# Optimization experiments

Hardware: AMD Instinct MI355X
Metric: run time of the kernel (lower is better)

## Reference

```python
import jax, jax.numpy as jnp
import numpy as np

B, S, D = 2, 2048, 1024
H, HD = 16, 64          # num_heads, head_dim
K = 32                  # JL n_components


def setup_inputs() -> dict:
    key = jax.random.key(0)
    k1, k2, k3, k4 = jax.random.split(key, 4)
    return {
        "hidden_states": jax.random.normal(k1, (B, S, D), dtype=jnp.float32),
        "W_attn": jax.random.normal(k2, (D, 3 * D), dtype=jnp.float32) * 0.02,
        "b_attn": jnp.zeros((3 * D,), dtype=jnp.float32),
        "S_proj": jax.random.normal(k3, (K, HD), dtype=jnp.float32) / np.sqrt(K),
        "W_proj": jax.random.normal(k4, (D, D), dtype=jnp.float32) * 0.02,
        "b_proj": jnp.zeros((D,), dtype=jnp.float32),
    }


def reference(hidden_states, W_attn, b_attn, S_proj, W_proj, b_proj):
    b, s, d = hidden_states.shape
    # GPT2 Conv1D: x @ W + b, then split into q,k,v
    qkv = hidden_states @ W_attn + b_attn            # [B,S,3D]
    q, k, v = jnp.split(qkv, 3, axis=-1)
    # split heads -> [B,H,S,HD]
    def split_heads(x):
        return x.reshape(b, s, H, HD).transpose(0, 2, 1, 3)
    q = split_heads(q) @ S_proj.T                    # [B,H,S,K] JL-reduced
    k = split_heads(k) @ S_proj.T                    # [B,H,S,K]
    v = split_heads(v)                               # [B,H,S,HD]
    # naive attention: scale by sqrt(value head_dim) per GPT2 _attn
    scores = jnp.einsum("bhqk,bhsk->bhqs", q, k) / jnp.sqrt(
        jnp.asarray(HD, dtype=v.dtype))              # [B,H,S,S]
    causal = jnp.tril(jnp.ones((s, s), dtype=bool))
    mask_value = jnp.finfo(scores.dtype).min
    scores = jnp.where(causal, scores, mask_value)
    attn = jax.nn.softmax(scores, axis=-1)
    out = jnp.einsum("bhqs,bhsd->bhqd", attn, v)     # [B,H,S,HD]
    out = out.transpose(0, 2, 1, 3).reshape(b, s, d)  # merge heads
    return out @ W_proj + b_proj
```

## Files before the change

### kernel.cpp

```cpp
#include <hip/hip_runtime.h>
#include <hip/hip_bf16.h>
#include <stdint.h>

#define B_ 2
#define S_ 2048
#define D_ 1024
#define H_ 16
#define HD_ 64
#define KJL 32
#define N3 3072
#define N2 2048

typedef __attribute__((ext_vector_type(8))) __bf16 bf16x8;
typedef __attribute__((ext_vector_type(4))) float floatx4;
typedef __attribute__((ext_vector_type(4))) short short4v;
typedef __attribute__((ext_vector_type(2))) unsigned int uint2v;

__device__ __forceinline__ unsigned short f2b(float x) {
  union { float f; unsigned u; } v; v.f = x;
  unsigned r = v.u + 0x7fffu + ((v.u >> 16) & 1u);
  return (unsigned short)(r >> 16);
}

__device__ __forceinline__ unsigned int pkbf(float lo, float hi) {
  union { float f; unsigned u; } a, b;
  a.f = lo; b.f = hi;
  return __builtin_amdgcn_perm(b.u + 0x8000u, a.u + 0x8000u, 0x07060302u);
}

__device__ __forceinline__ void async16(const void* g, void* l) {
  __builtin_amdgcn_global_load_lds((__attribute__((address_space(1))) void*)(g),
                                   (__attribute__((address_space(3))) void*)(l),
                                   16, 0, 0);
}

__global__ __launch_bounds__(256)
void prep_kernel(const float* __restrict__ hidden, unsigned short* __restrict__ hB,
                 const float* __restrict__ W_attn, const float* __restrict__ b_attn,
                 const float* __restrict__ Sp, const float* __restrict__ W_proj,
                 unsigned short* __restrict__ Bt2, unsigned short* __restrict__ WpT,
                 float* __restrict__ bias2) {
  __shared__ float shmem[2048];
  const int bid = blockIdx.x;
  const int tid = threadIdx.x;

  if (bid < 512) {
    const int n4 = (B_ * S_ * D_) / 4;
    int i = bid * 256 + tid;
    for (; i < n4; i += 512 * 256) {
      float4 v = *(const float4*)(hidden + 4 * (size_t)i);
      short4v o = {(short)f2b(v.x), (short)f2b(v.y), (short)f2b(v.z), (short)f2b(v.w)};
      *(short4v*)(hB + 4 * (size_t)i) = o;
    }
  } else if (bid < 2560) {
    const float* in;
    unsigned short* out;
    int Cs, local;
    if (bid < 1536) { local = bid - 512;  in = W_attn + 2048; out = Bt2 + 1024 * 1024; Cs = N3; }
    else            { local = bid - 1536; in = W_proj;        out = WpT;               Cs = D_; }
    float (*t)[33] = (float(*)[33])shmem;
    int c0 = (local & 31) * 32, r0 = (local >> 5) * 32;
    int tx = tid & 31, ty = tid >> 5;
    for (int j = 0; j < 32; j += 8)
      t[ty + j][tx] = in[(size_t)(r0 + ty + j) * Cs + c0 + tx];
    __syncthreads();
    for (int j = 0; j < 32; j += 8)
      out[(size_t)(c0 + ty + j) * D_ + r0 + tx] = f2b(t[tx][ty + j]);
  } else {
    const int lb = bid - 2560;
    const int part = lb >> 6;
    const int h = (lb >> 2) & 15;
    const int dc = lb & 3;
    for (int i = tid; i < 32 * 64; i += 256) shmem[i] = Sp[i];
    __syncthreads();
    const float scale = part ? 1.0f : 0.125f * 1.44269504f;
    const int d = dc * 256 + tid;
    float w[64];
    const float* src = W_attn + (size_t)d * N3 + part * D_ + h * 64;
    for (int j = 0; j < 16; ++j) {
      float4 v = *(const float4*)&src[j * 4];
      w[j * 4 + 0] = v.x; w[j * 4 + 1] = v.y; w[j * 4 + 2] = v.z; w[j * 4 + 3] = v.w;
    }
    const int nbase = part * 512 + h * 32;
    for (int kjl = 0; kjl < 32; ++kjl) {
      float acc = 0.f;
      for (int hd = 0; hd < 64; ++hd) acc += w[hd] * shmem[kjl * 64 + hd];
      Bt2[(size_t)(nbase + kjl) * D_ + d] = f2b(acc * scale);
    }
    if (dc == 0 && tid < 32) {
      float acc = 0.f;
      for (int hd = 0; hd < 64; ++hd) acc += b_attn[part * D_ + h * 64 + hd] * shmem[tid * 64 + hd];
      bias2[nbase + tid] = acc * scale;
    }
  }
}

__global__ __launch_bounds__(256, 2)
void qkv2_gemm_kernel(const unsigned short* __restrict__ A,
                      const unsigned short* __restrict__ Bt,
                      const float* __restrict__ b_attn,
                      const float* __restrict__ bias2,
                      unsigned short* __restrict__ Qjl,
                      unsigned short* __restrict__ Kjl,
                      unsigned short* __restrict__ Vc) {
  __shared__ __align__(16) unsigned short As[2][128 * 32];
  __shared__ __align__(16) unsigned short Bs[2][128 * 32];
  const int tid = threadIdx.x;
  const int lane = tid & 63, wv = tid >> 6;
  const int quad = lane >> 4, col = lane & 15;
  const int wm = wv >> 1, wn = wv & 1;
  const int m0 = blockIdx.y * 128, n0 = blockIdx.x * 128;

  floatx4 acc[4][4] = {};

  for (int kk = 0; kk < D_; kk += 64) {
    for (int it = 0; it < 4; ++it) {
      int c = it * 256 + tid;
      int ks = c >> 9, row = (c >> 2) & 127, kc = c & 3;
      async16(A + (size_t)(m0 + row) * D_ + kk + ks * 32 + kc * 8,
              (unsigned short*)As + c * 8);
    }
    for (int it = 0; it < 4; ++it) {
      int c = it * 256 + tid;
      int ks = c >> 9, row = (c >> 2) & 127, kc = c & 3;
      async16(Bt + (size_t)(n0 + row) * D_ + kk + ks * 32 + kc * 8,
              (unsigned short*)Bs + c * 8);
    }
    asm volatile("s_waitcnt vmcnt(0)" ::: "memory");
    __syncthreads();
    for (int ks = 0; ks < 2; ++ks) {
      bf16x8 af[4], bfr[4];
      for (int mt = 0; mt < 4; ++mt)
        af[mt] = *(const bf16x8*)&As[ks][(wm * 64 + mt * 16 + col) * 32 + quad * 8];
      for (int nt = 0; nt < 4; ++nt)
        bfr[nt] = *(const bf16x8*)&Bs[ks][(wn * 64 + nt * 16 + col) * 32 + quad * 8];
      for (int mt = 0; mt < 4; ++mt)
        for (int nt = 0; nt < 4; ++nt)
          acc[mt][nt] = __builtin_amdgcn_mfma_f32_16x16x32_bf16(
              af[mt], bfr[nt], acc[mt][nt], 0, 0, 0);
    }
    __syncthreads();
  }

  const int pq = n0 >> 9;
  for (int mt = 0; mt < 4; ++mt) {
    int gm0 = m0 + wm * 64 + mt * 16 + quad * 4;
    int b = gm0 >> 11, s = gm0 & (S_ - 1);
    for (int nt = 0; nt < 4; ++nt) {
      int gn = n0 + wn * 64 + nt * 16 + col;
      if (pq >= 2) {
        int vcol = gn - 1024;
        float bs = b_attn[2048 + vcol];
        int h = vcol >> 6, hd = vcol & 63;
        short4v vv;
        for (int i = 0; i < 4; ++i)
          vv[i] = (short)f2b(acc[mt][nt][i] + bs);
        size_t idx = ((((size_t)(b * H_ + h) * 64 + (s >> 5)) * 64 + hd) * 32 + (s & 31));
        *(short4v*)&Vc[idx] = vv;
      } else {
        float bs = bias2[gn];
        int gl = gn & 511;
        int h = gl >> 5, kjl = gl & 31;
        unsigned short* dst = pq ? Kjl : Qjl;
        size_t base = ((size_t)(b * H_ + h) * S_ + s) * KJL + kjl;
        for (int i = 0; i < 4; ++i)
          dst[base + (size_t)i * KJL] = f2b(acc[mt][nt][i] + bs);
      }
    }
  }
}

__global__ __launch_bounds__(256, 1)
void attn_kernel(const unsigned short* __restrict__ Qjl,
                 const unsigned short* __restrict__ Kjl,
                 const unsigned short* __restrict__ Vc,
                 unsigned short* __restrict__ AO) {
  __shared__ __align__(16) unsigned short Kb[3][4096];
  __shared__ __align__(16) unsigned short Vb[3][8192];
  __shared__ __align__(16) unsigned short Ps[4][4096];
  const int tid = threadIdx.x;
  const int lane = tid & 63, wv = tid >> 6;
  const int quad = lane >> 4, l15 = lane & 15;

  const int blk = blockIdx.x;
  const int bh = blk & 31;
  const int u = blk >> 5;
  const int b = bh >> 4, h = bh & 15;

  const unsigned short* Kg = Kjl + (size_t)bh * S_ * KJL;
  const unsigned short* Vg = Vc + (size_t)bh * (64 * 64 * 32);

  char* Pw = (char*)&Ps[wv][0];
  const int pswz = l15 << 4;
  const floatx4 zz = {0.f, 0.f, 0.f, 0.f};

#define STAGE(bu, c) do {                                                   \
    const char* ks_ = (const char*)(Kg + (size_t)(c) * 4096);               \
    const char* vs_ = (const char*)(Vg + (size_t)(c) * 8192);               \
    char* kd_ = (char*)&Kb[bu][0];                                          \
    char* vd_ = (char*)&Vb[bu][0];                                          \
    async16(ks_ + tid * 16,         kd_ + tid * 16);                        \
    async16(ks_ + tid * 16 + 4096,  kd_ + tid * 16 + 4096);                 \
    async16(vs_ + tid * 16,         vd_ + tid * 16);                        \
    async16(vs_ + tid * 16 + 4096,  vd_ + tid * 16 + 4096);                 \
    async16(vs_ + tid * 16 + 8192,  vd_ + tid * 16 + 8192);                 \
    async16(vs_ + tid * 16 + 12288, vd_ + tid * 16 + 12288);                \
  } while (0)

  for (int ph = 0; ph < 2; ++ph) {
    const int g = ph ? (15 - u) : u;
    const int t = g * 4 + wv;
    const int nch = g + 1;
    const int lastc = g;

    bf16x8 aq[2];
    for (int qn = 0; qn < 2; ++qn)
      aq[qn] = *(const bf16x8*)&Qjl[(size_t)(bh * S_ + t * 32 + qn * 16 + l15) * KJL + quad * 8];

    floatx4 o[4][2] = {};
    floatx4 psum[2] = {};

    STAGE(0, 0);
    if (nch > 1) {
      STAGE(1, 1);
      asm volatile("s_waitcnt vmcnt(6)" ::: "memory");
    } else {
      asm volatile("s_waitcnt vmcnt(0)" ::: "memory");
    }
    __builtin_amdgcn_s_barrier();

    for (int kt = 0; kt < nch; ++kt) {
      const int cur = kt % 3;
      if (kt + 2 < nch) STAGE((kt + 2) % 3, kt + 2);

      const char* Kc = (const char*)&Kb[cur][0];
      const char* Vl = (const char*)&Vb[cur][0];

      bf16x8 ak[8];
      for (int sm = 0; sm < 8; ++sm)
        ak[sm] = *(const bf16x8*)(Kc + (sm * 16 + l15) * 64 + quad * 16);

      floatx4 sc[8][2];
      __builtin_amdgcn_s_setprio(1);
      for (int sm = 0; sm < 8; ++sm)
        for (int qn = 0; qn < 2; ++qn)
          sc[sm][qn] = __builtin_amdgcn_mfma_f32_16x16x32_bf16(ak[sm], aq[qn], zz, 0, 0, 0);
      __builtin_amdgcn_s_setprio(0);

      if (kt == lastc) {
        for (int qn = 0; qn < 2; ++qn) {
          int qloc = wv * 32 + qn * 16 + l15;
          for (int sm = 0; sm < 8; ++sm)
            for (int i = 0; i < 4; ++i)
              if (sm * 16 + quad * 4 + i > qloc) sc[sm][qn][i] = -1e30f;
        }
      }

      for (int qn = 0; qn < 2; ++qn) {
        for (int sm = 0; sm < 8; ++sm) {
          float p0 = __builtin_amdgcn_exp2f(sc[sm][qn][0]);
          float p1 = __builtin_amdgcn_exp2f(sc[sm][qn][1]);
          float p2 = __builtin_amdgcn_exp2f(sc[sm][qn][2]);
          float p3 = __builtin_amdgcn_exp2f(sc[sm][qn][3]);
          psum[qn][0] += p0; psum[qn][1] += p1;
          psum[qn][2] += p2; psum[qn][3] += p3;
          uint2v pk2 = {pkbf(p0, p1), pkbf(p2, p3)};
          *(uint2v*)(Pw + (qn * 16 + l15) * 256 + ((sm * 32 + quad * 8) ^ pswz)) = pk2;
        }
      }

      for (int ks = 0; ks < 4; ++ks) {
        bf16x8 bv[4];
        for (int md = 0; md < 4; ++md)
          bv[md] = *(const bf16x8*)(Vl + ks * 4096 + md * 1024 + l15 * 64 + quad * 16);
        bf16x8 bp[2];
        for (int qn = 0; qn < 2; ++qn)
          bp[qn] = *(const bf16x8*)(Pw + (qn * 16 + l15) * 256 + ((ks * 64 + quad * 16) ^ pswz));
        __builtin_amdgcn_s_setprio(1);
        for (int qn = 0; qn < 2; ++qn)
          for (int md = 0; md < 4; ++md)
            o[md][qn] = __builtin_amdgcn_mfma_f32_16x16x32_bf16(bv[md], bp[qn], o[md][qn], 0, 0, 0);
        __builtin_amdgcn_s_setprio(0);
      }

      if (kt + 2 < nch) {
        asm volatile("s_waitcnt vmcnt(6)" ::: "memory");
      } else {
        asm volatile("s_waitcnt vmcnt(0)" ::: "memory");
      }
      __builtin_amdgcn_s_barrier();
    }

    float l0 = psum[0][0] + psum[0][1] + psum[0][2] + psum[0][3];
    float l1 = psum[1][0] + psum[1][1] + psum[1][2] + psum[1][3];
    l0 += __shfl_xor(l0, 16, 64); l0 += __shfl_xor(l0, 32, 64);
    l1 += __shfl_xor(l1, 16, 64); l1 += __shfl_xor(l1, 32, 64);

    {
      unsigned short* Pu = (unsigned short*)Pw;
      float inv0 = 1.f / l0;
      float inv1 = 1.f / l1;
      for (int qn = 0; qn < 2; ++qn) {
        float inv = qn ? inv1 : inv0;
        for (int md = 0; md < 4; ++md) {
          floatx4 s = o[md][qn];
          uint2v t4 = {pkbf(s[0] * inv, s[1] * inv),
                       pkbf(s[2] * inv, s[3] * inv)};
          *(uint2v*)&Pu[(qn * 16 + l15) * 72 + md * 16 + quad * 4] = t4;
        }
      }
      asm volatile("s_waitcnt lgkmcnt(0)" ::: "memory");
      int q = lane >> 1, hf = lane & 1;
      size_t gbase = ((size_t)(b * S_ + t * 32 + q)) * D_ + h * HD_ + hf * 32;
      for (int jj = 0; jj < 4; ++jj) {
        bf16x8 v = *(const bf16x8*)&Pu[q * 72 + hf * 32 + jj * 8];
        *(bf16x8*)&AO[gbase + jj * 8] = v;
      }
    }
  }
#undef STAGE
}

__global__ __launch_bounds__(256, 2)
void proj_gemm_kernel(const unsigned short* __restrict__ A,
                      const unsigned short* __restrict__ Bt,
                      const float* __restrict__ bias,
                      float* __restrict__ out) {
  __shared__ __align__(16) unsigned short As[2][64 * 32];
  __shared__ __align__(16) unsigned short Bs[2][128 * 32];
  const int tid = threadIdx.x;
  const int lane = tid & 63, wv = tid >> 6;
  const int quad = lane >> 4, col = lane & 15;
  const int wm = wv >> 1, wn = wv & 1;
  const int m0 = blockIdx.y * 64, n0 = blockIdx.x * 128;

  floatx4 acc[2][4] = {};

  for (int kk = 0; kk < D_; kk += 64) {
    for (int it = 0; it < 2; ++it) {
      int c = it * 256 + tid;
      int ks = c >> 8, row = (c >> 2) & 63, kc = c & 3;
      async16(A + (size_t)(m0 + row) * D_ + kk + ks * 32 + kc * 8,
              (unsigned short*)As + c * 8);
    }
    for (int it = 0; it < 4; ++it) {
      int c = it * 256 + tid;
      int ks = c >> 9, row = (c >> 2) & 127, kc = c & 3;
      async16(Bt + (size_t)(n0 + row) * D_ + kk + ks * 32 + kc * 8,
              (unsigned short*)Bs + c * 8);
    }
    asm volatile("s_waitcnt vmcnt(0)" ::: "memory");
    __syncthreads();
    for (int ks = 0; ks < 2; ++ks) {
      bf16x8 af[2], bfr[4];
      for (int mt = 0; mt < 2; ++mt)
        af[mt] = *(const bf16x8*)&As[ks][(wm * 32 + mt * 16 + col) * 32 + quad * 8];
      for (int nt = 0; nt < 4; ++nt)
        bfr[nt] = *(const bf16x8*)&Bs[ks][(wn * 64 + nt * 16 + col) * 32 + quad * 8];
      for (int mt = 0; mt < 2; ++mt)
        for (int nt = 0; nt < 4; ++nt)
          acc[mt][nt] = __builtin_amdgcn_mfma_f32_16x16x32_bf16(
              af[mt], bfr[nt], acc[mt][nt], 0, 0, 0);
    }
    __syncthreads();
  }

  for (int mt = 0; mt < 2; ++mt) {
    int gm0 = m0 + wm * 32 + mt * 16 + quad * 4;
    for (int nt = 0; nt < 4; ++nt) {
      int gn = n0 + wn * 64 + nt * 16 + col;
      float bs = bias[gn];
      for (int i = 0; i < 4; ++i)
        out[(size_t)(gm0 + i) * D_ + gn] = acc[mt][nt][i] + bs;
    }
  }
}

extern "C" void kernel_launch(void* const* d_in, const int* in_sizes, int n_in,
                              void* d_out, int out_size, void* d_ws, size_t ws_size,
                              hipStream_t stream) {
  (void)in_sizes; (void)n_in; (void)out_size; (void)ws_size;
  const float* hidden = (const float*)d_in[0];
  const float* W_attn = (const float*)d_in[1];
  const float* b_attn = (const float*)d_in[2];
  const float* S_proj = (const float*)d_in[3];
  const float* W_proj = (const float*)d_in[4];
  const float* b_proj = (const float*)d_in[5];
  float* out = (float*)d_out;

  char* ws = (char*)d_ws;
  unsigned short* hB    = (unsigned short*)(ws);
  unsigned short* Bt2   = (unsigned short*)(ws + (8u << 20));
  unsigned short* WpT   = (unsigned short*)(ws + (12u << 20));
  float*          bias2 = (float*)         (ws + (14u << 20));
  unsigned short* Qjl   = (unsigned short*)(ws + (15u << 20));
  unsigned short* Kjl   = (unsigned short*)(ws + (19u << 20));
  unsigned short* Vc    = (unsigned short*)(ws + (23u << 20));
  unsigned short* AO    = (unsigned short*)(ws + (31u << 20));

  prep_kernel<<<2688, 256, 0, stream>>>(hidden, hB, W_attn, b_attn, S_proj,
                                        W_proj, Bt2, WpT, bias2);
  qkv2_gemm_kernel<<<dim3(N2 / 128, (B_ * S_) / 128), 256, 0, stream>>>(
      hB, Bt2, b_attn, bias2, Qjl, Kjl, Vc);
  attn_kernel<<<256, 256, 0, stream>>>(Qjl, Kjl, Vc, AO);
  proj_gemm_kernel<<<dim3(D_ / 128, (B_ * S_) / 64), 256, 0, stream>>>(
      AO, WpT, b_proj, out);
}
```

Measured before the change: 182.6 us.

## Split attention block into 8 waves of 16 queries each

Doubles the attention block to 512 threads, with each wave handling 16 query rows instead of 32. Each block still covers 128 queries per phase. Staging K/V chunks is spread across twice as many threads, so each thread issues fewer async loads, and the output write is re-swizzled for the smaller per-wave tile. This aims for more waves per CU to hide latency, but each wave now reads K and V from LDS for only 16 queries, which doubles LDS read traffic per unit of work.

```diff
diff --git a/kernel.cpp b/kernel.cpp
--- a/kernel.cpp
+++ b/kernel.cpp
@@ -170,14 +170,14 @@
   }
 }
 
-__global__ __launch_bounds__(256, 1)
+__global__ __launch_bounds__(512, 1)
 void attn_kernel(const unsigned short* __restrict__ Qjl,
                  const unsigned short* __restrict__ Kjl,
                  const unsigned short* __restrict__ Vc,
                  unsigned short* __restrict__ AO) {
   __shared__ __align__(16) unsigned short Kb[3][4096];
   __shared__ __align__(16) unsigned short Vb[3][8192];
-  __shared__ __align__(16) unsigned short Ps[4][4096];
+  __shared__ __align__(16) unsigned short Ps[8][2048];
   const int tid = threadIdx.x;
   const int lane = tid & 63, wv = tid >> 6;
   const int quad = lane >> 4, l15 = lane & 15;
@@ -199,31 +199,26 @@
     const char* vs_ = (const char*)(Vg + (size_t)(c) * 8192);               \
     char* kd_ = (char*)&Kb[bu][0];                                          \
     char* vd_ = (char*)&Vb[bu][0];                                          \
-    async16(ks_ + tid * 16,         kd_ + tid * 16);                        \
-    async16(ks_ + tid * 16 + 4096,  kd_ + tid * 16 + 4096);                 \
-    async16(vs_ + tid * 16,         vd_ + tid * 16);                        \
-    async16(vs_ + tid * 16 + 4096,  vd_ + tid * 16 + 4096);                 \
-    async16(vs_ + tid * 16 + 8192,  vd_ + tid * 16 + 8192);                 \
-    async16(vs_ + tid * 16 + 12288, vd_ + tid * 16 + 12288);                \
+    async16(ks_ + tid * 16,        kd_ + tid * 16);                         \
+    async16(vs_ + tid * 16,        vd_ + tid * 16);                         \
+    async16(vs_ + tid * 16 + 8192, vd_ + tid * 16 + 8192);                  \
   } while (0)
 
   for (int ph = 0; ph < 2; ++ph) {
     const int g = ph ? (15 - u) : u;
-    const int t = g * 4 + wv;
+    const int t = g * 8 + wv;
     const int nch = g + 1;
     const int lastc = g;
 
-    bf16x8 aq[2];
-    for (int qn = 0; qn < 2; ++qn)
-      aq[qn] = *(const bf16x8*)&Qjl[(size_t)(bh * S_ + t * 32 + qn * 16 + l15) * KJL + quad * 8];
-
-    floatx4 o[4][2] = {};
-    floatx4 psum[2] = {};
+    bf16x8 aq = *(const bf16x8*)&Qjl[(size_t)(bh * S_ + t * 16 + l15) * KJL + quad * 8];
+
+    floatx4 o[4] = {};
+    floatx4 psum = {};
 
     STAGE(0, 0);
     if (nch > 1) {
       STAGE(1, 1);
-      asm volatile("s_waitcnt vmcnt(6)" ::: "memory");
+      asm volatile("s_waitcnt vmcnt(3)" ::: "memory");
     } else {
       asm volatile("s_waitcnt vmcnt(0)" ::: "memory");
     }
@@ -240,81 +235,66 @@
       for (int sm = 0; sm < 8; ++sm)
         ak[sm] = *(const bf16x8*)(Kc + (sm * 16 + l15) * 64 + quad * 16);
 
-      floatx4 sc[8][2];
+      floatx4 sc[8];
       __builtin_amdgcn_s_setprio(1);
       for (int sm = 0; sm < 8; ++sm)
-        for (int qn = 0; qn < 2; ++qn)
-          sc[sm][qn] = __builtin_amdgcn_mfma_f32_16x16x32_bf16(ak[sm], aq[qn], zz, 0, 0, 0);
+        sc[sm] = __builtin_amdgcn_mfma_f32_16x16x32_bf16(ak[sm], aq, zz, 0, 0, 0);
       __builtin_amdgcn_s_setprio(0);
 
       if (kt == lastc) {
-        for (int qn = 0; qn < 2; ++qn) {
-          int qloc = wv * 32 + qn * 16 + l15;
-          for (int sm = 0; sm < 8; ++sm)
-            for (int i = 0; i < 4; ++i)
-              if (sm * 16 + quad * 4 + i > qloc) sc[sm][qn][i] = -1e30f;
-        }
-      }
-
-      for (int qn = 0; qn < 2; ++qn) {
-        for (int sm = 0; sm < 8; ++sm) {
-          float p0 = __builtin_amdgcn_exp2f(sc[sm][qn][0]);
-          float p1 = __builtin_amdgcn_exp2f(sc[sm][qn][1]);
-          float p2 = __builtin_amdgcn_exp2f(sc[sm][qn][2]);
-          float p3 = __builtin_amdgcn_exp2f(sc[sm][qn][3]);
-          psum[qn][0] += p0; psum[qn][1] += p1;
-          psum[qn][2] += p2; psum[qn][3] += p3;
-          uint2v pk2 = {pkbf(p0, p1), pkbf(p2, p3)};
-          *(uint2v*)(Pw + (qn * 16 + l15) * 256 + ((sm * 32 + quad * 8) ^ pswz)) = pk2;
-        }
+        int qloc = wv * 16 + l15;
+        for (int sm = 0; sm < 8; ++sm)
+          for (int i = 0; i < 4; ++i)
+            if (sm * 16 + quad * 4 + i > qloc) sc[sm][i] = -1e30f;
+      }
+
+      for (int sm = 0; sm < 8; ++sm) {
+        float p0 = __builtin_amdgcn_exp2f(sc[sm][0]);
+        float p1 = __builtin_amdgcn_exp2f(sc[sm][1]);
+        float p2 = __builtin_amdgcn_exp2f(sc[sm][2]);
+        float p3 = __builtin_amdgcn_exp2f(sc[sm][3]);
+        psum[0] += p0; psum[1] += p1; psum[2] += p2; psum[3] += p3;
+        uint2v pk2 = {pkbf(p0, p1), pkbf(p2, p3)};
+        *(uint2v*)(Pw + l15 * 256 + ((sm * 32 + quad * 8) ^ pswz)) = pk2;
       }
 
       for (int ks = 0; ks < 4; ++ks) {
         bf16x8 bv[4];
         for (int md = 0; md < 4; ++md)
           bv[md] = *(const bf16x8*)(Vl + ks * 4096 + md * 1024 + l15 * 64 + quad * 16);
-        bf16x8 bp[2];
-        for (int qn = 0; qn < 2; ++qn)
-          bp[qn] = *(const bf16x8*)(Pw + (qn * 16 + l15) * 256 + ((ks * 64 + quad * 16) ^ pswz));
+        bf16x8 bp = *(const bf16x8*)(Pw + l15 * 256 + ((ks * 64 + quad * 16) ^ pswz));
         __builtin_amdgcn_s_setprio(1);
-        for (int qn = 0; qn < 2; ++qn)
-          for (int md = 0; md < 4; ++md)
-            o[md][qn] = __builtin_amdgcn_mfma_f32_16x16x32_bf16(bv[md], bp[qn], o[md][qn], 0, 0, 0);
+        for (int md = 0; md < 4; ++md)
+          o[md] = __builtin_amdgcn_mfma_f32_16x16x32_bf16(bv[md], bp, o[md], 0, 0, 0);
         __builtin_amdgcn_s_setprio(0);
       }
 
       if (kt + 2 < nch) {
-        asm volatile("s_waitcnt vmcnt(6)" ::: "memory");
+        asm volatile("s_waitcnt vmcnt(3)" ::: "memory");
       } else {
         asm volatile("s_waitcnt vmcnt(0)" ::: "memory");
       }
       __builtin_amdgcn_s_barrier();
     }
 
-    float l0 = psum[0][0] + psum[0][1] + psum[0][2] + psum[0][3];
-    float l1 = psum[1][0] + psum[1][1] + psum[1][2] + psum[1][3];
-    l0 += __shfl_xor(l0, 16, 64); l0 += __shfl_xor(l0, 32, 64);
-    l1 += __shfl_xor(l1, 16, 64); l1 += __shfl_xor(l1, 32, 64);
+    float l0 = psum[0] + psum[1] + psum[2] + psum[3];
+    l0 += __shfl_xor(l0, 16, 64);
+    l0 += __shfl_xor(l0, 32, 64);
+    float inv = 1.f / l0;
 
     {
-      unsigned short* Pu = (unsigned short*)Pw;
-      float inv0 = 1.f / l0;
-      float inv1 = 1.f / l1;
-      for (int qn = 0; qn < 2; ++qn) {
-        float inv = qn ? inv1 : inv0;
-        for (int md = 0; md < 4; ++md) {
-          floatx4 s = o[md][qn];
-          uint2v t4 = {pkbf(s[0] * inv, s[1] * inv),
-                       pkbf(s[2] * inv, s[3] * inv)};
-          *(uint2v*)&Pu[(qn * 16 + l15) * 72 + md * 16 + quad * 4] = t4;
-        }
+      const int eswz = (l15 & 7) << 4;
+      for (int md = 0; md < 4; ++md) {
+        uint2v t4 = {pkbf(o[md][0] * inv, o[md][1] * inv),
+                     pkbf(o[md][2] * inv, o[md][3] * inv)};
+        *(uint2v*)(Pw + l15 * 128 + ((md * 32 + quad * 8) ^ eswz)) = t4;
       }
       asm volatile("s_waitcnt lgkmcnt(0)" ::: "memory");
-      int q = lane >> 1, hf = lane & 1;
-      size_t gbase = ((size_t)(b * S_ + t * 32 + q)) * D_ + h * HD_ + hf * 32;
-      for (int jj = 0; jj < 4; ++jj) {
-        bf16x8 v = *(const bf16x8*)&Pu[q * 72 + hf * 32 + jj * 8];
-        *(bf16x8*)&AO[gbase + jj * 8] = v;
+      int q = lane >> 2, j = lane & 3;
+      size_t gbase = ((size_t)(b * S_ + t * 16 + q)) * D_ + h * HD_;
+      for (int half = 0; half < 2; ++half) {
+        bf16x8 v = *(const bf16x8*)(Pw + q * 128 + ((half * 64 + j * 16) ^ ((q & 7) << 4)));
+        *(bf16x8*)&AO[gbase + half * 32 + j * 8] = v;
       }
     }
   }
@@ -402,7 +382,7 @@
                                         W_proj, Bt2, WpT, bias2);
   qkv2_gemm_kernel<<<dim3(N2 / 128, (B_ * S_) / 128), 256, 0, stream>>>(
       hB, Bt2, b_attn, bias2, Qjl, Kjl, Vc);
-  attn_kernel<<<256, 256, 0, stream>>>(Qjl, Kjl, Vc, AO);
+  attn_kernel<<<256, 512, 0, stream>>>(Qjl, Kjl, Vc, AO);
   proj_gemm_kernel<<<dim3(D_ / 128, (B_ * S_) / 64), 256, 0, stream>>>(
       AO, WpT, b_proj, out);
 }
```

Result: no change. 179.2 us (-1.9%).
